# Kernel tuning notes

Measured on AMD Instinct MI355X. Metric: run time of the kernel, lower is better.

## Reference

```python
import jax, jax.numpy as jnp
import numpy as np

GAMMA = 2.6
SIG0, SIG1 = 0.17, 4.86
EXP_S, EXP_F = 2.0, 0.6

F1_NP = np.array([[0.0025, 0.0125, 0.02, 0.0125, 0.0025],
                  [0.0125, 0.0625, 0.1, 0.0625, 0.0125],
                  [0.02, 0.1, 0.16, 0.1, 0.02],
                  [0.0125, 0.0625, 0.1, 0.0625, 0.0125],
                  [0.0025, 0.0125, 0.02, 0.0125, 0.0025]], dtype=np.float32)[None, None]
FILT0_NP = np.array([[0.04, 0.04, 0.05, 0.04, 0.04],
                     [0.04, 0.03, 0.04, 0.03, 0.04],
                     [0.05, 0.04, 0.05, 0.04, 0.05],
                     [0.04, 0.03, 0.04, 0.03, 0.04],
                     [0.04, 0.04, 0.05, 0.04, 0.04]], dtype=np.float32)[None, None]
FILT1_NP = np.zeros((5, 5), dtype=np.float32)
FILT1_NP[2, 2] = 1.0
FILT1_NP = FILT1_NP[None, None]


def _pad_rep(x, p):
    return jnp.pad(x, ((0, 0), (0, 0), (p, p), (p, p)), mode='edge')


def _conv(x, f, pad=0):
    return jax.lax.conv_general_dilated(
        x, f, window_strides=(1, 1), padding=[(pad, pad), (pad, pad)],
        dimension_numbers=('NCHW', 'OIHW', 'NCHW'))


def _down(img, f):
    # replicate-pad by 2, valid 5x5 conv (output same HxW), stride-2 subsample
    o = _conv(_pad_rep(img, 2), f)
    return o[:, :, ::2, ::2]


def _up(img, odd, f):
    x = _pad_rep(img, 1)
    B, C, Hp, Wp = x.shape
    h, w = 2 * Hp, 2 * Wp
    o = jnp.zeros((B, C, h, w), x.dtype).at[:, :, ::2, ::2].set(4.0 * x)
    o = _conv(o, f, pad=2)
    return o[:, :, 2:h - 2 - odd[0], 2:w - 2 - odd[1]]


def _laplacian_pyramid(img, n_lev, f):
    pyr = []
    o = img
    for _ in range(n_lev - 1):
        g = _down(o, f)
        odd = [g.shape[2] * 2 - o.shape[2], g.shape[3] * 2 - o.shape[3]]
        pyr.append(o - _up(g, odd, f))
        o = g
    pyr.append(o)
    return pyr


def _nlp(img, n_lev, F1, filt0, filt1):
    img = img ** (1.0 / GAMMA)
    pyr = _laplacian_pyramid(img, n_lev, F1)
    npyr = []
    for i in range(n_lev - 1):
        den = _conv(_pad_rep(jnp.abs(pyr[i]), 2), filt0) + SIG0
        npyr.append(pyr[i] / den)
    den = _conv(_pad_rep(jnp.abs(pyr[-1]), 2), filt1) + SIG1
    npyr.append(pyr[-1] / den)
    return npyr


def setup_inputs() -> dict:
    key = jax.random.key(0)
    k1, k2 = jax.random.split(key)
    B, H, W = 16, 512, 512
    h_img = jax.random.uniform(k1, (B, 1, H, W), dtype=jnp.float32)
    l_img = jax.random.uniform(k2, (B, 1, H, W), dtype=jnp.float32)
    return {
        'h_img': h_img,
        'l_img': l_img,
        'F1': jnp.asarray(F1_NP),
        'filt0': jnp.asarray(FILT0_NP),
        'filt1': jnp.asarray(FILT1_NP),
        'n_lev': 7,
    }


def reference(h_img, l_img, F1, filt0, filt1, n_lev):
    h_pyr = _nlp(h_img, n_lev, F1, filt0, filt1)
    l_pyr = _nlp(l_img, n_lev, F1, filt0, filt1)
    dis = []
    for i in range(n_lev):
        diff = jnp.abs(h_pyr[i] - l_pyr[i]) ** EXP_S
        dis.append(jnp.mean(diff, axis=(-2, -1)) ** (EXP_F / EXP_S))  # [B, 1]
    dis = jnp.concatenate(dis, axis=-1)  # [B, n_lev]
    loss = jnp.mean(dis, axis=-1) ** (1.0 / EXP_F)
    return jnp.mean(loss)
```

## Files before the change

kernel.cpp:

```cpp
#include <hip/hip_runtime.h>

#define SIG0 0.17f
#define SIG1 4.86f

__device__ __constant__ float c_filt0[25] = {
  0.04f,0.04f,0.05f,0.04f,0.04f,
  0.04f,0.03f,0.04f,0.03f,0.04f,
  0.05f,0.04f,0.05f,0.04f,0.05f,
  0.04f,0.03f,0.04f,0.03f,0.04f,
  0.04f,0.04f,0.05f,0.04f,0.04f};
__device__ __constant__ float c_f1d[5] = {0.05f,0.25f,0.4f,0.25f,0.05f};

static __device__ __forceinline__ int iclamp(int v, int lo, int hi){
  return v < lo ? lo : (v > hi ? hi : v);
}


struct FS {
  float sg[2][20][76];
  float s1[2][12][44];
  float red[4];
};
struct DS {
  float st[20][136];
  float hs[20][64];
};
struct TS {
  float A3[2][64][66];
  float A4[2][32][34];
  float A5[2][16][18];
  float A6[2][8][10];
  float red[4];
};

__device__ __forceinline__ void down_body(const float* __restrict__ in0, float* __restrict__ out0,
                                          int PSI, int PSO, int Sout, int xo0, int yo0, char* smem){
  DS* S = (DS*)smem;
  int tid = threadIdx.x;
  for (int f=tid; f<20*34; f+=256){
    int r=f/34, c4=f-34*r;
    *(float4*)&S->st[r][4*c4] = *(const float4*)&in0[(size_t)(2*yo0+r)*PSI + 2*xo0 + 4*c4];
  }
  __syncthreads();
  for (int f=tid; f<20*64; f+=256){
    int r=f>>6, xo=f&63;
    const float* rp = &S->st[r][2*xo+2];
    S->hs[r][xo] = 0.05f*rp[0]+0.25f*rp[1]+0.4f*rp[2]+0.25f*rp[3]+0.05f*rp[4];
  }
  __syncthreads();
  for (int f=tid; f<8*64; f+=256){
    int yo=f>>6, xo=f&63;
    int Y=yo0+yo, X=xo0+xo;
    float v = 0.05f*S->hs[2*yo][xo]+0.25f*S->hs[2*yo+1][xo]+0.4f*S->hs[2*yo+2][xo]
            +0.25f*S->hs[2*yo+3][xo]+0.05f*S->hs[2*yo+4][xo];
    int rlo=(Y==0)?0:(Y+2), rhi=(Y==Sout-1)?(Sout+3):(Y+2);
    int clo=(X==0)?0:(X+4), chi=(X==Sout-1)?(Sout+7):(X+4);
    for (int rr=rlo; rr<=rhi; rr++)
      for (int cc=clo; cc<=chi; cc++)
        out0[(size_t)rr*PSO+cc] = v;
  }
}

__global__ __launch_bounds__(256)
void k_d1(const float* __restrict__ hin, const float* __restrict__ lin,
          float* __restrict__ g1){
  __shared__ DS S;
  int xo0 = blockIdx.x*64, yo0 = blockIdx.y*8, z = blockIdx.z;
  const float* in = (z<16)? hin + (size_t)z*262144 : lin + (size_t)(z-16)*262144;
  float* out0 = g1 + (size_t)z*68640;
  int tid = threadIdx.x;
  const float e = 0.3846153846153846f;
  for (int f=tid; f<20*34; f+=256){
    int r=f/34, c4=f-34*r;
    int yy = iclamp(2*yo0-2+r, 0, 511);
    int xb = 2*xo0-4+4*c4;
    const float* rp = in + (size_t)yy*512;
    float4 v;
    if (xb>=0 && xb<=508) v = *(const float4*)&rp[xb];
    else { v.x=rp[iclamp(xb,0,511)]; v.y=rp[iclamp(xb+1,0,511)];
           v.z=rp[iclamp(xb+2,0,511)]; v.w=rp[iclamp(xb+3,0,511)]; }
    v.x=__powf(v.x,e); v.y=__powf(v.y,e); v.z=__powf(v.z,e); v.w=__powf(v.w,e);
    *(float4*)&S.st[r][4*c4] = v;
  }
  __syncthreads();
  for (int f=tid; f<20*64; f+=256){
    int r=f>>6, xo=f&63;
    const float* rp = &S.st[r][2*xo+2];
    S.hs[r][xo] = 0.05f*rp[0]+0.25f*rp[1]+0.4f*rp[2]+0.25f*rp[3]+0.05f*rp[4];
  }
  __syncthreads();
  for (int f=tid; f<8*64; f+=256){
    int yo=f>>6, xo=f&63;
    int Y=yo0+yo, X=xo0+xo;
    float v = 0.05f*S.hs[2*yo][xo]+0.25f*S.hs[2*yo+1][xo]+0.4f*S.hs[2*yo+2][xo]
            +0.25f*S.hs[2*yo+3][xo]+0.05f*S.hs[2*yo+4][xo];
    int rlo=(Y==0)?0:(Y+2), rhi=(Y==255)?259:(Y+2);
    int clo=(X==0)?0:(X+4), chi=(X==255)?263:(X+4);
    for (int rr=rlo; rr<=rhi; rr++)
      for (int cc=clo; cc<=chi; cc++)
        out0[(size_t)rr*264+cc] = v;
  }
}

template<int GAMMA>
__device__ __forceinline__ void fused_body(FS* S,
    const float* __restrict__ a0, const float* __restrict__ a1, int PS0,
    const float* __restrict__ s10, const float* __restrict__ s11, int PS1,
    int Simg, int x0, int y0, float* __restrict__ out_slot){
  int t = threadIdx.x;
  const float e = 0.3846153846153846f;

  if (t < 240){
    int img = t >= 120; int t2 = img ? t-120 : t;
    int r = t2/6, q3 = t2 - 6*r;
    float4 w0, w1, w2;
    if (GAMMA){
      int yy = iclamp(y0-2+r, 0, 511);
      int xb = x0-4+12*q3;
      const float* rp = (img ? a1 : a0) + (size_t)yy*512;
      if (xb >= 0 && xb <= 500){
        w0 = *(const float4*)&rp[xb];
        w1 = *(const float4*)&rp[xb+4];
        w2 = *(const float4*)&rp[xb+8];
      } else {
        w0.x=rp[iclamp(xb+0,0,511)];  w0.y=rp[iclamp(xb+1,0,511)];
        w0.z=rp[iclamp(xb+2,0,511)];  w0.w=rp[iclamp(xb+3,0,511)];
        w1.x=rp[iclamp(xb+4,0,511)];  w1.y=rp[iclamp(xb+5,0,511)];
        w1.z=rp[iclamp(xb+6,0,511)];  w1.w=rp[iclamp(xb+7,0,511)];
        w2.x=rp[iclamp(xb+8,0,511)];  w2.y=rp[iclamp(xb+9,0,511)];
        w2.z=rp[iclamp(xb+10,0,511)]; w2.w=rp[iclamp(xb+11,0,511)];
      }
      w0.x=__powf(w0.x,e); w0.y=__powf(w0.y,e); w0.z=__powf(w0.z,e); w0.w=__powf(w0.w,e);
      w1.x=__powf(w1.x,e); w1.y=__powf(w1.y,e); w1.z=__powf(w1.z,e); w1.w=__powf(w1.w,e);
      w2.x=__powf(w2.x,e); w2.y=__powf(w2.y,e); w2.z=__powf(w2.z,e); w2.w=__powf(w2.w,e);
    } else {
      const float* rp = (img ? a1 : a0) + (size_t)(y0+r)*PS0 + x0 + 12*q3;
      w0 = *(const float4*)&rp[0];
      w1 = *(const float4*)&rp[4];
      w2 = *(const float4*)&rp[8];
    }
    float* dp = &S->sg[img][r][12*q3];
    *(float4*)&dp[0] = w0;
    *(float4*)&dp[4] = w1;
    *(float4*)&dp[8] = w2;
  }
  if (t < 240){
    int img = t >= 120; int t2 = img ? t-120 : t;
    int ro = t2/10, co = t2 - 10*ro;
    const float* src = (img ? s11 : s10) + (size_t)(y0/2+ro)*PS1 + x0/2 + 4*co;
    *(float4*)&S->s1[img][ro][4*co] = *(const float4*)src;
  }
  __syncthreads();

  if (t < 180){
    int img = t >= 90; int t2 = img ? t-90 : t;
    int rp_ = t2/9, q = t2 - 9*rp_;
    int cb1 = 4*q, cbg = 8*q;
    float4 Aa = *(const float4*)&S->s1[img][rp_  ][cb1];
    float4 Ab = *(const float4*)&S->s1[img][rp_  ][cb1+4];
    float4 Ba = *(const float4*)&S->s1[img][rp_+1][cb1];
    float4 Bb = *(const float4*)&S->s1[img][rp_+1][cb1+4];
    float4 Ca = *(const float4*)&S->s1[img][rp_+2][cb1];
    float4 Cb = *(const float4*)&S->s1[img][rp_+2][cb1+4];
    float hEA0=0.05f*Aa.y+0.4f*Aa.z+0.05f*Aa.w, hOA0=0.25f*(Aa.z+Aa.w);
    float hEA1=0.05f*Aa.z+0.4f*Aa.w+0.05f*Ab.x, hOA1=0.25f*(Aa.w+Ab.x);
    float hEA2=0.05f*Aa.w+0.4f*Ab.x+0.05f*Ab.y, hOA2=0.25f*(Ab.x+Ab.y);
    float hEA3=0.05f*Ab.x+0.4f*Ab.y+0.05f*Ab.z, hOA3=0.25f*(Ab.y+Ab.z);
    float hEB0=0.05f*Ba.y+0.4f*Ba.z+0.05f*Ba.w, hOB0=0.25f*(Ba.z+Ba.w);
    float hEB1=0.05f*Ba.z+0.4f*Ba.w+0.05f*Bb.x, hOB1=0.25f*(Ba.w+Bb.x);
    float hEB2=0.05f*Ba.w+0.4f*Bb.x+0.05f*Bb.y, hOB2=0.25f*(Bb.x+Bb.y);
    float hEB3=0.05f*Bb.x+0.4f*Bb.y+0.05f*Bb.z, hOB3=0.25f*(Bb.y+Bb.z);
    float hEC0=0.05f*Ca.y+0.4f*Ca.z+0.05f*Ca.w, hOC0=0.25f*(Ca.z+Ca.w);
    float hEC1=0.05f*Ca.z+0.4f*Ca.w+0.05f*Cb.x, hOC1=0.25f*(Ca.w+Cb.x);
    float hEC2=0.05f*Ca.w+0.4f*Cb.x+0.05f*Cb.y, hOC2=0.25f*(Cb.x+Cb.y);
    float hEC3=0.05f*Cb.x+0.4f*Cb.y+0.05f*Cb.z, hOC3=0.25f*(Cb.y+Cb.z);
    float4 ue0, ue1, uo0, uo1;
    ue0.x=0.2f*hEA0+1.6f*hEB0+0.2f*hEC0;  ue0.y=0.2f*hOA0+1.6f*hOB0+0.2f*hOC0;
    ue0.z=0.2f*hEA1+1.6f*hEB1+0.2f*hEC1;  ue0.w=0.2f*hOA1+1.6f*hOB1+0.2f*hOC1;
    ue1.x=0.2f*hEA2+1.6f*hEB2+0.2f*hEC2;  ue1.y=0.2f*hOA2+1.6f*hOB2+0.2f*hOC2;
    ue1.z=0.2f*hEA3+1.6f*hEB3+0.2f*hEC3;  ue1.w=0.2f*hOA3+1.6f*hOB3+0.2f*hOC3;
    uo0.x=hEB0+hEC0;  uo0.y=hOB0+hOC0;  uo0.z=hEB1+hEC1;  uo0.w=hOB1+hOC1;
    uo1.x=hEB2+hEC2;  uo1.y=hOB2+hOC2;  uo1.z=hEB3+hEC3;  uo1.w=hOB3+hOC3;
    float* dpe = &S->sg[img][2*rp_][cbg];
    float4 v0 = *(float4*)&dpe[0];
    float4 v1 = *(float4*)&dpe[4];
    v0.x-=ue0.x; v0.y-=ue0.y; v0.z-=ue0.z; v0.w-=ue0.w;
    v1.x-=ue1.x; v1.y-=ue1.y; v1.z-=ue1.z; v1.w-=ue1.w;
    *(float4*)&dpe[0] = v0; *(float4*)&dpe[4] = v1;
    float* dpo = &S->sg[img][2*rp_+1][cbg];
    float4 u0 = *(float4*)&dpo[0];
    float4 u1 = *(float4*)&dpo[4];
    u0.x-=uo0.x; u0.y-=uo0.y; u0.z-=uo0.z; u0.w-=uo0.w;
    u1.x-=uo1.x; u1.y-=uo1.y; u1.z-=uo1.z; u1.w-=uo1.w;
    *(float4*)&dpo[0] = u0; *(float4*)&dpo[4] = u1;
  }
  __syncthreads();

  bool top=(y0==0), bot=(y0+16==Simg), lft=(x0==0), rgt=(x0+64==Simg);
  if (top|bot|lft|rgt){
    for (int f=t; f<2*18; f+=256){
      int img = f>=18; int q = img ? f-18 : f;
      if (top){ float4 v=*(float4*)&S->sg[img][2][4*q];
                *(float4*)&S->sg[img][0][4*q]=v; *(float4*)&S->sg[img][1][4*q]=v; }
      if (bot){ float4 v=*(float4*)&S->sg[img][17][4*q];
                *(float4*)&S->sg[img][18][4*q]=v; *(float4*)&S->sg[img][19][4*q]=v; }
    }
    __syncthreads();
    for (int f=t; f<2*20; f+=256){
      int img = f>=20; int r = img ? f-20 : f;
      if (lft){ float v=S->sg[img][r][4];  float4 vv={v,v,v,v}; *(float4*)&S->sg[img][r][0]=vv; }
      if (rgt){ float v=S->sg[img][r][67]; float4 vv={v,v,v,v}; *(float4*)&S->sg[img][r][68]=vv; }
    }
    __syncthreads();
  }

  float vacc = 0.f;
  {
    int img = t & 1, quad = t >> 1;
    int qx = quad & 15, qy = quad >> 4;
    int cb = 4*qx, rb = 2*qy;
    float4 Tq0={0,0,0,0}, Tq1={0,0,0,0};
    float4 s5a={0,0,0,0}, s5b={0,0,0,0}, s3a={0,0,0,0}, s3b={0,0,0,0};
    float4 n0={0,0,0,0}, n1={0,0,0,0};
    #pragma unroll
    for (int r=0;r<6;r++){
      const float* rp = &S->sg[img][rb+r][cb];
      float4 t0 = *(const float4*)&rp[0];
      float4 t1 = *(const float4*)&rp[4];
      float4 t2 = *(const float4*)&rp[8];
      float aw0=fabsf(t0.z), aw1=fabsf(t0.w), aw2=fabsf(t1.x), aw3=fabsf(t1.y);
      float aw4=fabsf(t1.z), aw5=fabsf(t1.w), aw6=fabsf(t2.x), aw7=fabsf(t2.y);
      float h0 = ((aw0+aw1)+(aw2+aw3))+aw4;
      float h1 = h0 - aw0 + aw5;
      float h2 = h1 - aw1 + aw6;
      float h3 = h2 - aw2 + aw7;
      if (r<=4){ Tq0.x+=h0; Tq0.y+=h1; Tq0.z+=h2; Tq0.w+=h3; }
      if (r>=1){ Tq1.x+=h0; Tq1.y+=h1; Tq1.z+=h2; Tq1.w+=h3; }
      if (r==0){ s5a.x=aw2; s5a.y=aw3; s5a.z=aw4; s5a.w=aw5; }
      if (r==1){
        s3a.x=aw1+aw3; s3a.y=aw2+aw4; s3a.z=aw3+aw5; s3a.w=aw4+aw6;
        s5b.x=aw2; s5b.y=aw3; s5b.z=aw4; s5b.w=aw5;
      }
      if (r==2){
        s5a.x+=aw0+aw2+aw4; s5a.y+=aw1+aw3+aw5; s5a.z+=aw2+aw4+aw6; s5a.w+=aw3+aw5+aw7;
        n0 = t1;
        s3b.x=aw1+aw3; s3b.y=aw2+aw4; s3b.z=aw3+aw5; s3b.w=aw4+aw6;
      }
      if (r==3){
        s3a.x+=aw1+aw3; s3a.y+=aw2+aw4; s3a.z+=aw3+aw5; s3a.w+=aw4+aw6;
        s5b.x+=aw0+aw2+aw4; s5b.y+=aw1+aw3+aw5; s5b.z+=aw2+aw4+aw6; s5b.w+=aw3+aw5+aw7;
        n1 = t1;
      }
      if (r==4){
        s5a.x+=aw2; s5a.y+=aw3; s5a.z+=aw4; s5a.w+=aw5;
        s3b.x+=aw1+aw3; s3b.y+=aw2+aw4; s3b.z+=aw3+aw5; s3b.w+=aw4+aw6;
      }
      if (r==5){ s5b.x+=aw2; s5b.y+=aw3; s5b.z+=aw4; s5b.w+=aw5; }
    }
    float q0 = __fdividef(n0.x, SIG0 + 0.04f*Tq0.x + 0.01f*s5a.x - 0.01f*s3a.x);
    float q1 = __fdividef(n0.y, SIG0 + 0.04f*Tq0.y + 0.01f*s5a.y - 0.01f*s3a.y);
    float q2 = __fdividef(n0.z, SIG0 + 0.04f*Tq0.z + 0.01f*s5a.z - 0.01f*s3a.z);
    float q3v= __fdividef(n0.w, SIG0 + 0.04f*Tq0.w + 0.01f*s5a.w - 0.01f*s3a.w);
    float q4 = __fdividef(n1.x, SIG0 + 0.04f*Tq1.x + 0.01f*s5b.x - 0.01f*s3b.x);
    float q5 = __fdividef(n1.y, SIG0 + 0.04f*Tq1.y + 0.01f*s5b.y - 0.01f*s3b.y);
    float q6 = __fdividef(n1.z, SIG0 + 0.04f*Tq1.z + 0.01f*s5b.z - 0.01f*s3b.z);
    float q7 = __fdividef(n1.w, SIG0 + 0.04f*Tq1.w + 0.01f*s5b.w - 0.01f*s3b.w);
    float d0 = q0 - __shfl_xor(q0, 1);
    float d1 = q1 - __shfl_xor(q1, 1);
    float d2 = q2 - __shfl_xor(q2, 1);
    float d3 = q3v- __shfl_xor(q3v, 1);
    float d4 = q4 - __shfl_xor(q4, 1);
    float d5 = q5 - __shfl_xor(q5, 1);
    float d6 = q6 - __shfl_xor(q6, 1);
    float d7 = q7 - __shfl_xor(q7, 1);
    vacc = ((d0*d0+d1*d1)+(d2*d2+d3*d3)) + ((d4*d4+d5*d5)+(d6*d6+d7*d7));
    if (t & 1) vacc = 0.f;
  }
  #pragma unroll
  for (int off=32; off>0; off>>=1) vacc += __shfl_down(vacc, off);
  if ((t&63)==0) S->red[t>>6] = vacc;
  __syncthreads();
  if (t==0)
    out_slot[0] = S->red[0]+S->red[1]+S->red[2]+S->red[3];
}

static __device__ __forceinline__ void down_lds(const float* Ain, int ldi, int Sin,
                                                float* Aout, int ldo, int Sout,
                                                int tid, int NT){
  int tot = 2*Sout*Sout;
  for (int f=tid; f<tot; f+=NT){
    int img = f/(Sout*Sout), rem = f%(Sout*Sout), y=rem/Sout, x=rem%Sout;
    const float* A = Ain + img*Sin*ldi;
    float s=0.f;
    #pragma unroll
    for (int i=0;i<5;i++){
      int yy=iclamp(2*y+i-2,0,Sin-1);
      float rs=0.f;
      #pragma unroll
      for (int j=0;j<5;j++){
        int xx=iclamp(2*x+j-2,0,Sin-1);
        rs += c_f1d[j]*A[yy*ldi+xx];
      }
      s += c_f1d[i]*rs;
    }
    Aout[img*Sout*ldo + y*ldo + x] = s;
  }
}

static __device__ __forceinline__ void lap_lds(float* Ak, int ldk, int S,
                                               const float* Ag, int ldg,
                                               int tid, int NT){
  int Sg = S>>1;
  int tot = 2*S*S;
  for (int f=tid; f<tot; f+=NT){
    int img=f/(S*S), rem=f%(S*S), y=rem/S, x=rem%S;
    const float* G = Ag + img*Sg*ldg;
    int y2=y>>1, x2=x>>1;
    int ry0,ry1,ry2; float wy0,wy1,wy2;
    if (!(y&1)){ ry0=iclamp(y2-1,0,Sg-1); ry1=y2; ry2=iclamp(y2+1,0,Sg-1); wy0=0.2f; wy1=1.6f; wy2=0.2f; }
    else { ry0=y2; ry1=iclamp(y2+1,0,Sg-1); ry2=y2; wy0=1.f; wy1=1.f; wy2=0.f; }
    int cx0,cx1,cx2; float wx0,wx1,wx2;
    if (!(x&1)){ cx0=iclamp(x2-1,0,Sg-1); cx1=x2; cx2=iclamp(x2+1,0,Sg-1); wx0=0.05f; wx1=0.4f; wx2=0.05f; }
    else { cx0=x2; cx1=iclamp(x2+1,0,Sg-1); cx2=x2; wx0=0.25f; wx1=0.25f; wx2=0.f; }
    float u0 = wx0*G[ry0*ldg+cx0]+wx1*G[ry0*ldg+cx1]+wx2*G[ry0*ldg+cx2];
    float u1 = wx0*G[ry1*ldg+cx0]+wx1*G[ry1*ldg+cx1]+wx2*G[ry1*ldg+cx2];
    float u2 = wx0*G[ry2*ldg+cx0]+wx1*G[ry2*ldg+cx1]+wx2*G[ry2*ldg+cx2];
    Ak[img*S*ldk + y*ldk + x] -= wy0*u0+wy1*u1+wy2*u2;
  }
}

static __device__ __forceinline__ float diff_lds(const float* A, int ld, int S,
                                                 int tid, int NT){
  float v=0.f;
  const float* Ah = A;
  const float* Al = A + S*ld;
  for (int f=tid; f<S*S; f+=NT){
    int y=f/S, x=f%S;
    float dh=SIG0, dl=SIG0;
    #pragma unroll
    for (int i=0;i<5;i++){
      int yy=iclamp(y+i-2,0,S-1);
      #pragma unroll
      for (int j=0;j<5;j++){
        int xx=iclamp(x+j-2,0,S-1);
        float w=c_filt0[i*5+j];
        dh += w*fabsf(Ah[yy*ld+xx]);
        dl += w*fabsf(Al[yy*ld+xx]);
      }
    }
    float d = __fdividef(Ah[y*ld+x],dh) - __fdividef(Al[y*ld+x],dl);
    v += d*d;
  }
  return v;
}

__device__ void tail_body(const float* __restrict__ g3, float* __restrict__ accum,
                          int b, char* smem){
  TS* T = (TS*)smem;
  int tid = threadIdx.x;
  const float* s0  = g3 + (size_t)b*4896 + 148;
  const float* s1p = g3 + (size_t)(b+16)*4896 + 148;
  for (int f=tid; f<2*4096; f+=256){
    int img=f>>12, rem=f&4095, r=rem>>6, c=rem&63;
    T->A3[img][r][c] = (img? s1p : s0)[(size_t)r*72+c];
  }
  __syncthreads();
  down_lds(&T->A3[0][0][0],66,64,&T->A4[0][0][0],34,32,tid,256);
  __syncthreads();
  down_lds(&T->A4[0][0][0],34,32,&T->A5[0][0][0],18,16,tid,256);
  __syncthreads();
  down_lds(&T->A5[0][0][0],18,16,&T->A6[0][0][0],10,8,tid,256);
  __syncthreads();
  lap_lds(&T->A3[0][0][0],66,64,&T->A4[0][0][0],34,tid,256);
  __syncthreads();
  float v3 = diff_lds(&T->A3[0][0][0],66,64,tid,256);
  lap_lds(&T->A4[0][0][0],34,32,&T->A5[0][0][0],18,tid,256);
  __syncthreads();
  float v4 = diff_lds(&T->A4[0][0][0],34,32,tid,256);
  lap_lds(&T->A5[0][0][0],18,16,&T->A6[0][0][0],10,tid,256);
  __syncthreads();
  float v5 = diff_lds(&T->A5[0][0][0],18,16,tid,256);
  float v6 = 0.f;
  for (int f=tid; f<64; f+=256){
    float ch = T->A6[0][f>>3][f&7];
    float cl = T->A6[1][f>>3][f&7];
    float d = __fdividef(ch, fabsf(ch)+SIG1) - __fdividef(cl, fabsf(cl)+SIG1);
    v6 += d*d;
  }
  float vs0=v3, vs1=v4, vs2=v5, vs3=v6;
  #pragma unroll
  for (int k=0;k<4;k++){
    float v = (k==0)?vs0:((k==1)?vs1:((k==2)?vs2:vs3));
    #pragma unroll
    for (int off=32; off>0; off>>=1) v += __shfl_down(v, off);
    if ((tid&63)==0) T->red[tid>>6] = v;
    __syncthreads();
    if (tid==0)
      accum[(3+k)*16 + b] = T->red[0]+T->red[1]+T->red[2]+T->red[3];
    __syncthreads();
  }
}

__global__ __launch_bounds__(256)
void k_d2(const float* __restrict__ h, const float* __restrict__ l,
          const float* __restrict__ g1, float* __restrict__ g2,
          float* __restrict__ p0){
  extern __shared__ char smem[];
  if (blockIdx.z < 16){
    int b = blockIdx.z, x0 = blockIdx.x*64, y0 = blockIdx.y*16;
    fused_body<1>((FS*)smem, h+(size_t)b*262144, l+(size_t)b*262144, 0,
                  g1+(size_t)b*68640, g1+(size_t)(b+16)*68640, 264,
                  512, x0, y0, p0 + b*256 + blockIdx.y*8 + blockIdx.x);
  } else {
    int id = (blockIdx.z-16)*256 + blockIdx.y*8 + blockIdx.x;
    int img = id>>5, rem = id&31, xt = rem&1, yt = rem>>1;
    down_body(g1+(size_t)img*68640, g2+(size_t)img*17952, 264, 136, 128, xt*64, yt*8, smem);
  }
}

__global__ __launch_bounds__(256)
void k_d4(const float* __restrict__ g1, float* __restrict__ g2,
          float* __restrict__ g3, float* __restrict__ p1){
  extern __shared__ char smem[];
  if (blockIdx.z < 16){
    int b = blockIdx.z, x0 = blockIdx.x*64, y0 = blockIdx.y*16;
    fused_body<0>((FS*)smem, g1+(size_t)b*68640, g1+(size_t)(b+16)*68640, 264,
                  g2+(size_t)b*17952, g2+(size_t)(b+16)*17952, 136,
                  256, x0, y0, p1 + b*64 + blockIdx.y*4 + blockIdx.x);
  } else {
    int id = (blockIdx.z-16)*64 + blockIdx.y*4 + blockIdx.x;
    int img = id>>3, yt = id&7;
    down_body(g2+(size_t)img*17952, g3+(size_t)img*4896, 136, 72, 64, 0, yt*8, smem);
  }
}

__global__ __launch_bounds__(256)
void k_d5(const float* __restrict__ g2, const float* __restrict__ g3,
          float* __restrict__ p2, float* __restrict__ accum){
  extern __shared__ char smem[];
  if (blockIdx.z < 16){
    int b = blockIdx.z, x0 = blockIdx.x*64, y0 = blockIdx.y*16;
    fused_body<0>((FS*)smem, g2+(size_t)b*17952, g2+(size_t)(b+16)*17952, 136,
                  g3+(size_t)b*4896, g3+(size_t)(b+16)*4896, 72,
                  128, x0, y0, p2 + b*16 + blockIdx.y*2 + blockIdx.x);
  } else {
    int id = blockIdx.y*2 + blockIdx.x;
    tail_body(g3, accum, id, smem);
  }
}

__global__ __launch_bounds__(256)
void k_d6(const float* __restrict__ p0, const float* __restrict__ p1,
          const float* __restrict__ p2, const float* __restrict__ accum,
          float* __restrict__ out){
  __shared__ float r0[16][16];
  __shared__ float r1[16][4];
  __shared__ float r2[16];
  __shared__ float fin[16];
  int t = threadIdx.x;
  {
    int b = t>>4, c = t&15;
    float s = 0.f;
    #pragma unroll
    for (int j=0;j<16;j++) s += p0[b*256 + c*16 + j];
    r0[b][c] = s;
  }
  if (t < 64){
    int b = t>>2, c = t&3;
    float s = 0.f;
    #pragma unroll
    for (int j=0;j<16;j++) s += p1[b*64 + c*16 + j];
    r1[b][c] = s;
  }
  if (t < 16){
    float s = 0.f;
    #pragma unroll
    for (int j=0;j<16;j++) s += p2[t*16 + j];
    r2[t] = s;
  }
  __syncthreads();
  if (t < 16){
    int b = t;
    float a0 = 0.f;
    #pragma unroll
    for (int c=0;c<16;c++) a0 += r0[b][c];
    float a1 = (r1[b][0]+r1[b][1])+(r1[b][2]+r1[b][3]);
    float a2 = r2[b];
    float m = powf(a0*(1.0f/262144.0f), 0.3f)
            + powf(a1*(1.0f/65536.0f), 0.3f)
            + powf(a2*(1.0f/16384.0f), 0.3f);
    #pragma unroll
    for (int k=3;k<7;k++){
      int hw = (512>>k)*(512>>k);
      m += powf(accum[k*16+b]/(float)hw, 0.3f);
    }
    m *= (1.0f/7.0f);
    fin[b] = powf(m, 1.6666666666666667f);
  }
  __syncthreads();
  if (t == 0){
    float s = 0.f;
    #pragma unroll
    for (int i=0;i<16;i++) s += fin[i];
    out[0] = s * (1.0f/16.0f);
  }
}

extern "C" void kernel_launch(void* const* d_in, const int* in_sizes, int n_in,
                              void* d_out, int out_size, void* d_ws, size_t ws_size,
                              hipStream_t stream){
  const float* h = (const float*)d_in[0];
  const float* l = (const float*)d_in[1];
  float* out = (float*)d_out;
  float* ws = (float*)d_ws;

  float* g1 = ws;
  float* g2 = g1 + 2196480;
  float* g3 = g2 + 574464;
  float* accum = g3 + 156672;
  float* p0 = accum + 112;
  float* p1 = p0 + 4096;
  float* p2 = p1 + 1024;

  size_t fsz = sizeof(FS) > sizeof(DS) ? sizeof(FS) : sizeof(DS);
  size_t tsz = sizeof(TS);

  k_d1<<<dim3(4,32,32), 256, 0, stream>>>(h, l, g1);
  k_d2<<<dim3(8,32,20), 256, fsz, stream>>>(h, l, g1, g2, p0);
  k_d4<<<dim3(4,16,20), 256, fsz, stream>>>(g1, g2, g3, p1);
  k_d5<<<dim3(2,8,17),  256, tsz, stream>>>(g2, g3, p2, accum);
  k_d6<<<1, 256, 0, stream>>>(p0, p1, p2, accum, out);
}
```

Baseline: 158.1 us.

## Move replicate-padding writes into separate pad kernels and enlarge d1 row tile

The downsample kernels no longer write the replicate-padded border inline through per-thread nested loops with branchy edge cases. Each now writes only its interior pixel, and three small k_pad kernels fill the edge columns and rows of g1, g2 and g3 afterwards. k_d1 also processes 16 output rows per block instead of 8, which cuts the overlapping halo reloads and the repeated pow on them at the cost of more shared memory. The trade is three extra kernel launches, each with only 32 blocks, against simpler and more uniform stores in the main kernels.

```diff
diff --git a/kernel.cpp b/kernel.cpp
--- a/kernel.cpp
+++ b/kernel.cpp
@@ -25,6 +25,10 @@
   float st[20][136];
   float hs[20][64];
 };
+struct D1 {
+  float st[36][136];
+  float hs[36][64];
+};
 struct TS {
   float A3[2][64][66];
   float A4[2][32][34];
@@ -33,6 +37,30 @@
   float red[4];
 };
 
+template<int S>
+__global__ __launch_bounds__(256)
+void k_pad(float* __restrict__ g){
+  constexpr int PS = S+8;
+  float* p = g + (size_t)blockIdx.x * (size_t)((S+4)*PS);
+  int t = threadIdx.x;
+  for (int f=t; f<S; f+=256){
+    int r = 2+f;
+    float lv = p[(size_t)r*PS+4], rv = p[(size_t)r*PS+S+3];
+    float4 l4={lv,lv,lv,lv}, r4={rv,rv,rv,rv};
+    *(float4*)&p[(size_t)r*PS+0]   = l4;
+    *(float4*)&p[(size_t)r*PS+S+4] = r4;
+  }
+  __syncthreads();
+  for (int f=t; f<PS/4; f+=256){
+    float4 v2 = *(const float4*)&p[(size_t)2*PS+4*f];
+    *(float4*)&p[(size_t)0*PS+4*f] = v2;
+    *(float4*)&p[(size_t)1*PS+4*f] = v2;
+    float4 vS = *(const float4*)&p[(size_t)(S+1)*PS+4*f];
+    *(float4*)&p[(size_t)(S+2)*PS+4*f] = vS;
+    *(float4*)&p[(size_t)(S+3)*PS+4*f] = vS;
+  }
+}
+
 __device__ __forceinline__ void down_body(const float* __restrict__ in0, float* __restrict__ out0,
                                           int PSI, int PSO, int Sout, int xo0, int yo0, char* smem){
   DS* S = (DS*)smem;
@@ -50,27 +78,22 @@
   __syncthreads();
   for (int f=tid; f<8*64; f+=256){
     int yo=f>>6, xo=f&63;
-    int Y=yo0+yo, X=xo0+xo;
     float v = 0.05f*S->hs[2*yo][xo]+0.25f*S->hs[2*yo+1][xo]+0.4f*S->hs[2*yo+2][xo]
             +0.25f*S->hs[2*yo+3][xo]+0.05f*S->hs[2*yo+4][xo];
-    int rlo=(Y==0)?0:(Y+2), rhi=(Y==Sout-1)?(Sout+3):(Y+2);
-    int clo=(X==0)?0:(X+4), chi=(X==Sout-1)?(Sout+7):(X+4);
-    for (int rr=rlo; rr<=rhi; rr++)
-      for (int cc=clo; cc<=chi; cc++)
-        out0[(size_t)rr*PSO+cc] = v;
+    out0[(size_t)(yo0+yo+2)*PSO + xo0+xo+4] = v;
   }
 }
 
 __global__ __launch_bounds__(256)
 void k_d1(const float* __restrict__ hin, const float* __restrict__ lin,
           float* __restrict__ g1){
-  __shared__ DS S;
-  int xo0 = blockIdx.x*64, yo0 = blockIdx.y*8, z = blockIdx.z;
+  __shared__ D1 S;
+  int xo0 = blockIdx.x*64, yo0 = blockIdx.y*16, z = blockIdx.z;
   const float* in = (z<16)? hin + (size_t)z*262144 : lin + (size_t)(z-16)*262144;
   float* out0 = g1 + (size_t)z*68640;
   int tid = threadIdx.x;
   const float e = 0.3846153846153846f;
-  for (int f=tid; f<20*34; f+=256){
+  for (int f=tid; f<36*34; f+=256){
     int r=f/34, c4=f-34*r;
     int yy = iclamp(2*yo0-2+r, 0, 511);
     int xb = 2*xo0-4+4*c4;
@@ -83,22 +106,17 @@
     *(float4*)&S.st[r][4*c4] = v;
   }
   __syncthreads();
-  for (int f=tid; f<20*64; f+=256){
+  for (int f=tid; f<36*64; f+=256){
     int r=f>>6, xo=f&63;
     const float* rp = &S.st[r][2*xo+2];
     S.hs[r][xo] = 0.05f*rp[0]+0.25f*rp[1]+0.4f*rp[2]+0.25f*rp[3]+0.05f*rp[4];
   }
   __syncthreads();
-  for (int f=tid; f<8*64; f+=256){
+  for (int f=tid; f<16*64; f+=256){
     int yo=f>>6, xo=f&63;
-    int Y=yo0+yo, X=xo0+xo;
     float v = 0.05f*S.hs[2*yo][xo]+0.25f*S.hs[2*yo+1][xo]+0.4f*S.hs[2*yo+2][xo]
             +0.25f*S.hs[2*yo+3][xo]+0.05f*S.hs[2*yo+4][xo];
-    int rlo=(Y==0)?0:(Y+2), rhi=(Y==255)?259:(Y+2);
-    int clo=(X==0)?0:(X+4), chi=(X==255)?263:(X+4);
-    for (int rr=rlo; rr<=rhi; rr++)
-      for (int cc=clo; cc<=chi; cc++)
-        out0[(size_t)rr*264+cc] = v;
+    out0[(size_t)(yo0+yo+2)*264 + xo0+xo+4] = v;
   }
 }
 
@@ -525,9 +543,12 @@
   size_t fsz = sizeof(FS) > sizeof(DS) ? sizeof(FS) : sizeof(DS);
   size_t tsz = sizeof(TS);
 
-  k_d1<<<dim3(4,32,32), 256, 0, stream>>>(h, l, g1);
+  k_d1<<<dim3(4,16,32), 256, 0, stream>>>(h, l, g1);
+  k_pad<256><<<32, 256, 0, stream>>>(g1);
   k_d2<<<dim3(8,32,20), 256, fsz, stream>>>(h, l, g1, g2, p0);
+  k_pad<128><<<32, 256, 0, stream>>>(g2);
   k_d4<<<dim3(4,16,20), 256, fsz, stream>>>(g1, g2, g3, p1);
+  k_pad<64><<<32, 256, 0, stream>>>(g3);
   k_d5<<<dim3(2,8,17),  256, tsz, stream>>>(g2, g3, p2, accum);
   k_d6<<<1, 256, 0, stream>>>(p0, p1, p2, accum, out);
 }
```

Result: no change. 160.7 us (+1.7%).
